# Kernel tuning notes

Measured on AMD Instinct MI355X. Metric: run time of the kernel, lower is better.

Reference implementation:

```python
import jax, jax.numpy as jnp
import numpy as np
import math

B, S, D, H = 2, 2048, 1024, 16
DK = D // H


def setup_inputs() -> dict:
    key = jax.random.key(0)
    ks = jax.random.split(key, 12)
    std = 1.0 / math.sqrt(D)
    inp = {
        "query": jax.random.normal(ks[0], (B, S, D), jnp.float32),
        "key": jax.random.normal(ks[1], (B, S, D), jnp.float32),
        "value": jax.random.normal(ks[2], (B, S, D), jnp.float32),
        # causal mask, broadcast over batch and heads
        "mask": jnp.tril(jnp.ones((S, S), jnp.int32))[None, None, :, :],
        # nn.Linear weights are [out_features, in_features]
        "Wq": jax.random.uniform(ks[3], (D, D), jnp.float32, -std, std),
        "bq": jax.random.uniform(ks[4], (D,), jnp.float32, -std, std),
        "Wk": jax.random.uniform(ks[5], (D, D), jnp.float32, -std, std),
        "bk": jax.random.uniform(ks[6], (D,), jnp.float32, -std, std),
        "Wv": jax.random.uniform(ks[7], (D, D), jnp.float32, -std, std),
        "bv": jax.random.uniform(ks[8], (D,), jnp.float32, -std, std),
        "Wo": jax.random.uniform(ks[9], (D, D), jnp.float32, -std, std),
        "bo": jax.random.uniform(ks[10], (D,), jnp.float32, -std, std),
    }
    return inp


def reference(query, key, value, mask, Wq, bq, Wk, bk, Wv, bv, Wo, bo):
    q = query @ Wq.T + bq  # [B,S,D]
    k = key @ Wk.T + bk
    v = value @ Wv.T + bv
    # Faithful to the original: a raw view (reshape), NOT a head-transpose split.
    q = q.reshape(B, H, S, DK)
    k = k.reshape(B, H, S, DK)
    v = v.reshape(B, H, S, DK)
    scores = jnp.einsum("bhqd,bhkd->bhqk", q, k) / math.sqrt(DK)
    scores = jnp.where(mask == 0, jnp.float32(-1e9), scores)
    weights = jax.nn.softmax(scores, axis=-1)
    # dropout(p=0.1) is identity in eval mode
    context = jnp.einsum("bhqk,bhkd->bhqd", weights, v)
    context = context.transpose(0, 2, 1, 3).reshape(B, S, D)
    return context @ Wo.T + bo
```

## Files before the change

### kernel.cpp

```cpp
#include <hip/hip_runtime.h>
#include <hip/hip_bf16.h>

#define BB 2
#define SS 2048
#define DD 1024
#define HH 16
#define DKK 64

typedef __attribute__((ext_vector_type(4))) float  f32x4;
typedef __attribute__((ext_vector_type(8))) short  s16x8;
typedef __attribute__((ext_vector_type(4))) short  s16x4;
typedef __attribute__((ext_vector_type(4))) float  fvec4;
typedef __attribute__((ext_vector_type(2))) unsigned int u32x2;
typedef __attribute__((ext_vector_type(4))) unsigned int u32x4;

__device__ __forceinline__ short f2bs(float f) {
    union { __hip_bfloat16 b; short s; } u;
    u.b = __float2bfloat16(f);
    return u.s;
}

__device__ __forceinline__ unsigned cvtpk(float lo, float hi) {
    unsigned r;
    asm("v_cvt_pk_bf16_f32 %0, %1, %2" : "=v"(r) : "v"(lo), "v"(hi));
    return r;
}

__device__ __forceinline__ void gload_lds16(const short* g, short* l) {
    __builtin_amdgcn_global_load_lds((const __attribute__((address_space(1))) void*)g,
                                     (__attribute__((address_space(3))) void*)l, 16, 0, 0);
}

__global__ __launch_bounds__(256) void cvt_w(
    const float* __restrict__ wq, const float* __restrict__ wk,
    const float* __restrict__ wv, const float* __restrict__ wo,
    short* __restrict__ wqo, short* __restrict__ wko,
    short* __restrict__ wvo, short* __restrict__ woo)
{
    const float* src; short* dst;
    switch (blockIdx.y) {
        case 0: src = wq; dst = wqo; break;
        case 1: src = wk; dst = wko; break;
        case 2: src = wv; dst = wvo; break;
        default: src = wo; dst = woo; break;
    }
    const int n = DD * DD;
    int i = (blockIdx.x * 256 + threadIdx.x) * 8;
    const int stride = gridDim.x * 256 * 8;
    for (; i < n; i += stride) {
        fvec4 a = *(const fvec4*)&src[i];
        fvec4 b = *(const fvec4*)&src[i + 4];
        s16x8 o;
        o[0] = f2bs(a[0]); o[1] = f2bs(a[1]); o[2] = f2bs(a[2]); o[3] = f2bs(a[3]);
        o[4] = f2bs(b[0]); o[5] = f2bs(b[1]); o[6] = f2bs(b[2]); o[7] = f2bs(b[3]);
        *(s16x8*)&dst[i] = o;
    }
}

template<int BN, int NXSH, bool OUTF32, bool AF32>
__global__ __launch_bounds__(256) void gemm_nt_v2(
    const void* __restrict__ A0, const void* __restrict__ A1, const void* __restrict__ A2,
    const short* __restrict__ B0, const short* __restrict__ B1, const short* __restrict__ B2,
    const float* __restrict__ c0, const float* __restrict__ c1, const float* __restrict__ c2,
    void* __restrict__ O0, void* __restrict__ O1, void* __restrict__ O2,
    float os0, float os1, float os2,
    int ppx, int NY, int KL, int N, int K)
{
    const int d   = blockIdx.x;
    const int xcd = d & 7;
    const int s   = d >> 3;
    const int x   = s & ((1 << NXSH) - 1);
    const int pl  = s >> NXSH;
    const int panel = xcd * ppx + pl;
    const int y   = panel % NY;
    const int z   = panel / NY;

    const void* Av    = z == 0 ? A0 : (z == 1 ? A1 : A2);
    const short* Bw   = z == 0 ? B0 : (z == 1 ? B1 : B2);
    const float* bias = z == 0 ? c0 : (z == 1 ? c1 : c2);
    void* Cp          = z == 0 ? O0 : (z == 1 ? O1 : O2);
    const float oscale = z == 0 ? os0 : (z == 1 ? os1 : os2);
    const short* Ab = (const short*)Av;
    const float* Af = (const float*)Av;

    __shared__ short As[128][64];
    __shared__ short Bs[BN][64];

    const int tid  = threadIdx.x;
    const int lane = tid & 63;
    const int wid  = tid >> 6;
    const int r16  = lane & 15;
    const int g    = lane >> 4;
    const int m0   = y * 128;
    const int n0   = x * BN;
    constexpr int MR = 4;
    constexpr int NR = BN / 32;
    const int wr   = (wid >> 1) * 64;
    const int wc   = (wid & 1) * (BN / 2);
    const int srow8 = lane >> 3;
    const int c8    = lane & 7;

    f32x4 acc[MR][NR];
#pragma unroll
    for (int mi = 0; mi < MR; ++mi)
#pragma unroll
        for (int ni = 0; ni < NR; ++ni) acc[mi][ni] = (f32x4){0.f, 0.f, 0.f, 0.f};

    const int csrc = (c8 ^ srow8) * 8;
    const int nk = KL >> 6;
#pragma unroll 1
    for (int kt = 0; kt < nk; ++kt) {
        const int k0 = kt * 64;
        if (kt) __syncthreads();
#pragma unroll
        for (int q = 0; q < BN / 32; ++q) {
            const int r = wid * (BN / 4) + q * 8 + srow8;
            gload_lds16(&Bw[(size_t)(n0 + r) * K + k0 + csrc], &Bs[wid * (BN / 4) + q * 8][0]);
        }
        if constexpr (AF32) {
#pragma unroll
            for (int it = 0; it < 4; ++it) {
                const int idx = it * 256 + tid;
                const int row = idx >> 3;
                const int ca  = idx & 7;
                const float* srcp = &Af[(size_t)(m0 + row) * K + k0 + ca * 8];
                const fvec4 a0 = *(const fvec4*)srcp;
                const fvec4 a1 = *(const fvec4*)(srcp + 4);
                u32x4 wv_;
                wv_[0] = cvtpk(a0[0], a0[1]);
                wv_[1] = cvtpk(a0[2], a0[3]);
                wv_[2] = cvtpk(a1[0], a1[1]);
                wv_[3] = cvtpk(a1[2], a1[3]);
                *(u32x4*)&As[row][((ca ^ (row & 7)) & 7) * 8] = wv_;
            }
        } else {
#pragma unroll
            for (int q = 0; q < 4; ++q) {
                const int r = wid * 32 + q * 8 + srow8;
                gload_lds16(&Ab[(size_t)(m0 + r) * K + k0 + csrc], &As[wid * 32 + q * 8][0]);
            }
        }
        __syncthreads();

#pragma unroll
        for (int kk = 0; kk < 2; ++kk) {
            s16x8 af[MR], bf[NR];
#pragma unroll
            for (int mi = 0; mi < MR; ++mi) {
                const int row = wr + mi * 16 + r16;
                af[mi] = *(const s16x8*)&As[row][((kk * 4 + g) ^ (row & 7)) * 8];
            }
#pragma unroll
            for (int ni = 0; ni < NR; ++ni) {
                const int row = wc + ni * 16 + r16;
                bf[ni] = *(const s16x8*)&Bs[row][((kk * 4 + g) ^ (row & 7)) * 8];
            }
#pragma unroll
            for (int mi = 0; mi < MR; ++mi)
#pragma unroll
                for (int ni = 0; ni < NR; ++ni)
                    acc[mi][ni] = __builtin_amdgcn_mfma_f32_16x16x32_bf16(
                        bf[ni], af[mi], acc[mi][ni], 0, 0, 0);
        }
    }

#pragma unroll
    for (int mi = 0; mi < MR; ++mi) {
        const size_t row = (size_t)(m0 + wr + mi * 16 + r16);
#pragma unroll
        for (int ni = 0; ni < NR; ++ni) {
            const int colb = n0 + wc + ni * 16 + g * 4;
            fvec4 bv;
            if (bias) bv = *(const fvec4*)&bias[colb];
            else      bv = (fvec4){0.f, 0.f, 0.f, 0.f};
            const f32x4 a = acc[mi][ni];
            const float v0 = (a[0] + bv[0]) * oscale;
            const float v1 = (a[1] + bv[1]) * oscale;
            const float v2 = (a[2] + bv[2]) * oscale;
            const float v3 = (a[3] + bv[3]) * oscale;
            if constexpr (OUTF32) {
                fvec4 o; o[0] = v0; o[1] = v1; o[2] = v2; o[3] = v3;
                *(fvec4*)&((float*)Cp)[row * N + colb] = o;
            } else {
                u32x2 w;
                w[0] = cvtpk(v0, v1);
                w[1] = cvtpk(v2, v3);
                *(u32x2*)&((short*)Cp)[row * N + colb] = w;
            }
        }
    }
}

__global__ __launch_bounds__(256) void mha_transpose_v(
    const short* __restrict__ vp, short* __restrict__ vT)
{
    const int st = blockIdx.x;
    const int bh = blockIdx.y;
    const short* src = vp + (size_t)bh * SS * DKK;
    short*       dst = vT + (size_t)bh * SS * DKK;
    const int tid = threadIdx.x;
#pragma unroll
    for (int i = 0; i < 2; ++i) {
        const int c  = tid + i * 256;
        const int dk = c >> 3;
        const int sc = c & 7;
        const int s0 = st * 64 + sc * 8;
        s16x8 v;
#pragma unroll
        for (int j = 0; j < 8; ++j) v[j] = src[(size_t)(s0 + j) * DKK + dk];
        *(s16x8*)&dst[(size_t)dk * SS + s0] = v;
    }
}

__global__ __launch_bounds__(256, 2) void mha_attn(
    const short* __restrict__ qp, const short* __restrict__ kp,
    const short* __restrict__ vT, short* __restrict__ ctx)
{
    __shared__ short Ks[64][64];
    __shared__ short Vs[64][64];
    __shared__ short P[4][16][72];

    const int tid  = threadIdx.x;
    const int wid  = tid >> 6;
    const int lane = tid & 63;
    const int r16  = lane & 15;
    const int g    = lane >> 4;

    const int lin = blockIdx.x;
    const int xcd = lin & 7;
    const int s8  = lin >> 3;
    const int bh  = (xcd << 2) | (s8 & 3);
    const int v   = s8 >> 2;
    const int grp = (v < 16) ? v : (47 - v);
    const int b   = bh >> 4;
    const int h   = bh & 15;

    const short* Qh = qp + (size_t)bh * SS * DKK;
    const short* Kh = kp + (size_t)bh * SS * DKK;
    const short* Vh = vT + (size_t)bh * SS * DKK;

    const int srow = lane >> 3;
    const int csw  = (((lane & 7) ^ srow) & 7) * 8;
    const int r0   = wid * 16;

    const int qr0 = grp * 64 + wid * 16;
    const int nkt = grp + 1;

    const s16x8 qf0 = *(const s16x8*)&Qh[(size_t)(qr0 + r16) * DKK + g * 8];
    const s16x8 qf1 = *(const s16x8*)&Qh[(size_t)(qr0 + r16) * DKK + 32 + g * 8];

    f32x4 po[4];
#pragma unroll
    for (int i = 0; i < 4; ++i) po[i] = (f32x4){0.f, 0.f, 0.f, 0.f};
    float lsum = 0.f;

#pragma unroll 1
    for (int j = 0; j < nkt; ++j) {
        const int k0 = j * 64;
        __syncthreads();
        {
            const int rowA = r0 + srow;
            const int rowB = rowA + 8;
            gload_lds16(&Kh[(size_t)(k0 + rowA) * DKK + csw], &Ks[r0][0]);
            gload_lds16(&Kh[(size_t)(k0 + rowB) * DKK + csw], &Ks[r0 + 8][0]);
            gload_lds16(&Vh[(size_t)rowA * SS + k0 + csw], &Vs[r0][0]);
            gload_lds16(&Vh[(size_t)rowB * SS + k0 + csw], &Vs[r0 + 8][0]);
        }
        __syncthreads();

        f32x4 sc[4];
        __builtin_amdgcn_s_setprio(1);
#pragma unroll
        for (int cg = 0; cg < 4; ++cg) {
            const int R  = cg * 16 + r16;
            const int sw = R & 7;
            const s16x8 kf0 = *(const s16x8*)&Ks[R][((g ^ sw) & 7) * 8];
            const s16x8 kf1 = *(const s16x8*)&Ks[R][(((4 + g) ^ sw) & 7) * 8];
            f32x4 tt = (f32x4){0.f, 0.f, 0.f, 0.f};
            tt = __builtin_amdgcn_mfma_f32_16x16x32_bf16(kf0, qf0, tt, 0, 0, 0);
            tt = __builtin_amdgcn_mfma_f32_16x16x32_bf16(kf1, qf1, tt, 0, 0, 0);
            sc[cg] = tt;
        }
        __builtin_amdgcn_s_setprio(0);

        if (j == nkt - 1) {
#pragma unroll
            for (int cg = 0; cg < 4; ++cg)
#pragma unroll
                for (int r = 0; r < 4; ++r)
                    if (k0 + cg * 16 + g * 4 + r > qr0 + r16) sc[cg][r] = -1e9f;
        }
#pragma unroll
        for (int cg = 0; cg < 4; ++cg) {
            const float p0 = __expf(sc[cg][0]);
            const float p1 = __expf(sc[cg][1]);
            const float p2 = __expf(sc[cg][2]);
            const float p3 = __expf(sc[cg][3]);
            lsum += (p0 + p1) + (p2 + p3);
            u32x2 w;
            w[0] = cvtpk(p0, p1);
            w[1] = cvtpk(p2, p3);
            *(u32x2*)&P[wid][r16][cg * 16 + g * 4] = w;
        }
        const s16x8 pf0 = *(const s16x8*)&P[wid][r16][g * 8];
        const s16x8 pf1 = *(const s16x8*)&P[wid][r16][32 + g * 8];

        __builtin_amdgcn_s_setprio(1);
#pragma unroll
        for (int dg = 0; dg < 4; ++dg) {
            const int Rv = dg * 16 + r16;
            const int sw = Rv & 7;
            const s16x8 vf0 = *(const s16x8*)&Vs[Rv][((g ^ sw) & 7) * 8];
            const s16x8 vf1 = *(const s16x8*)&Vs[Rv][(((4 + g) ^ sw) & 7) * 8];
            po[dg] = __builtin_amdgcn_mfma_f32_16x16x32_bf16(pf0, vf0, po[dg], 0, 0, 0);
            po[dg] = __builtin_amdgcn_mfma_f32_16x16x32_bf16(pf1, vf1, po[dg], 0, 0, 0);
        }
        __builtin_amdgcn_s_setprio(0);
    }

    lsum += __shfl_xor(lsum, 16);
    lsum += __shfl_xor(lsum, 32);
    const float linv = __builtin_amdgcn_rcpf(lsum);
    float rowinv[4];
#pragma unroll
    for (int r = 0; r < 4; ++r)
        rowinv[r] = __shfl(linv, g * 4 + r);
#pragma unroll
    for (int dg = 0; dg < 4; ++dg)
#pragma unroll
        for (int r = 0; r < 4; ++r) {
            const int srw = qr0 + g * 4 + r;
            const float vv = po[dg][r] * rowinv[r];
            ctx[((size_t)(b * SS + srw)) * DD + h * 64 + dg * 16 + r16] = f2bs(vv);
        }
}

extern "C" void kernel_launch(void* const* d_in, const int* in_sizes, int n_in,
                              void* d_out, int out_size, void* d_ws, size_t ws_size,
                              hipStream_t stream) {
    const float* query = (const float*)d_in[0];
    const float* key   = (const float*)d_in[1];
    const float* value = (const float*)d_in[2];
    const float* Wq = (const float*)d_in[4];
    const float* bq = (const float*)d_in[5];
    const float* Wk = (const float*)d_in[6];
    const float* bk = (const float*)d_in[7];
    const float* Wv = (const float*)d_in[8];
    const float* bv = (const float*)d_in[9];
    const float* Wo = (const float*)d_in[10];
    const float* bo = (const float*)d_in[11];
    float* out = (float*)d_out;

    const size_t elems = (size_t)BB * SS * DD;
    const size_t wel   = (size_t)DD * DD;
    short* wqx = (short*)d_ws;
    short* wkx = wqx + wel;
    short* wvx = wkx + wel;
    short* wox = wvx + wel;
    short* qp  = wox + wel;
    short* kp  = qp + elems;
    short* vp  = kp + elems;
    short* vT  = vp + elems;
    short* ctx = vT + elems;

    cvt_w<<<dim3(512, 4), 256, 0, stream>>>(Wq, Wk, Wv, Wo, wqx, wkx, wvx, wox);
    gemm_nt_v2<128, 3, false, true><<<dim3(768), 256, 0, stream>>>(
        query, key, value, wqx, wkx, wvx, bq, bk, bv, qp, kp, vp,
        0.125f, 1.0f, 1.0f, 12, 32, 1024, DD, DD);
    mha_transpose_v<<<dim3(SS / 64, BB * HH), 256, 0, stream>>>(vp, vT);
    mha_attn<<<dim3(1024), 256, 0, stream>>>(qp, kp, vT, ctx);
    gemm_nt_v2<64, 4, true, false><<<dim3(512), 256, 0, stream>>>(
        ctx, ctx, ctx, wox, wox, wox, bo, bo, bo, out, out, out,
        1.0f, 1.0f, 1.0f, 4, 32, 1024, DD, DD);
}
```

Before: 114.2 us.

## Prefetch next fp32 A tile into registers during MFMA in projection GEMM

In the fp32-input GEMM path, global loads of the next K-tile of A are issued before the current tile's MFMA work, and the bf16 conversion runs after it. This overlaps global latency with compute instead of stalling on loads each iteration. The syncthreads calls are replaced by manual waitcnt and s_barrier calls with sched barriers, which adds register pressure and relies on the vmcnt counting being correct.

```diff
diff --git a/kernel.cpp b/kernel.cpp
--- a/kernel.cpp
+++ b/kernel.cpp
@@ -108,59 +108,126 @@
 
     const int csrc = (c8 ^ srow8) * 8;
     const int nk = KL >> 6;
+
+    if constexpr (AF32) {
+        const int brow = tid >> 3;
+        const int ca   = tid & 7;
+        const int cswA = ((ca ^ (brow & 7)) & 7) * 8;
+
+        fvec4 la0[4], la1[4];
+        u32x4 areg[4];
+
+#pragma unroll
+        for (int it = 0; it < 4; ++it) {
+            const float* sp = &Af[(size_t)(m0 + brow + it * 32) * K + ca * 8];
+            la0[it] = *(const fvec4*)sp;
+            la1[it] = *(const fvec4*)(sp + 4);
+        }
+#pragma unroll
+        for (int it = 0; it < 4; ++it) {
+            areg[it][0] = cvtpk(la0[it][0], la0[it][1]);
+            areg[it][1] = cvtpk(la0[it][2], la0[it][3]);
+            areg[it][2] = cvtpk(la1[it][0], la1[it][1]);
+            areg[it][3] = cvtpk(la1[it][2], la1[it][3]);
+        }
+
 #pragma unroll 1
-    for (int kt = 0; kt < nk; ++kt) {
-        const int k0 = kt * 64;
-        if (kt) __syncthreads();
-#pragma unroll
-        for (int q = 0; q < BN / 32; ++q) {
-            const int r = wid * (BN / 4) + q * 8 + srow8;
-            gload_lds16(&Bw[(size_t)(n0 + r) * K + k0 + csrc], &Bs[wid * (BN / 4) + q * 8][0]);
-        }
-        if constexpr (AF32) {
-#pragma unroll
-            for (int it = 0; it < 4; ++it) {
-                const int idx = it * 256 + tid;
-                const int row = idx >> 3;
-                const int ca  = idx & 7;
-                const float* srcp = &Af[(size_t)(m0 + row) * K + k0 + ca * 8];
-                const fvec4 a0 = *(const fvec4*)srcp;
-                const fvec4 a1 = *(const fvec4*)(srcp + 4);
-                u32x4 wv_;
-                wv_[0] = cvtpk(a0[0], a0[1]);
-                wv_[1] = cvtpk(a0[2], a0[3]);
-                wv_[2] = cvtpk(a1[0], a1[1]);
-                wv_[3] = cvtpk(a1[2], a1[3]);
-                *(u32x4*)&As[row][((ca ^ (row & 7)) & 7) * 8] = wv_;
-            }
-        } else {
+        for (int kt = 0; kt < nk; ++kt) {
+            const int k0 = kt * 64;
+#pragma unroll
+            for (int it = 0; it < 4; ++it)
+                *(u32x4*)&As[brow + it * 32][cswA] = areg[it];
+#pragma unroll
+            for (int q = 0; q < BN / 32; ++q) {
+                const int r = wid * (BN / 4) + q * 8 + srow8;
+                gload_lds16(&Bw[(size_t)(n0 + r) * K + k0 + csrc], &Bs[wid * (BN / 4) + q * 8][0]);
+            }
+            const bool hasNext = (kt + 1 < nk);
+            if (hasNext) {
+                const int k1 = k0 + 64;
+#pragma unroll
+                for (int it = 0; it < 4; ++it) {
+                    const float* sp = &Af[(size_t)(m0 + brow + it * 32) * K + k1 + ca * 8];
+                    la0[it] = *(const fvec4*)sp;
+                    la1[it] = *(const fvec4*)(sp + 4);
+                }
+                asm volatile("s_waitcnt vmcnt(8) lgkmcnt(0)" ::: "memory");
+            } else {
+                asm volatile("s_waitcnt vmcnt(0) lgkmcnt(0)" ::: "memory");
+            }
+            __builtin_amdgcn_s_barrier();
+            __builtin_amdgcn_sched_barrier(0);
+
+#pragma unroll
+            for (int kk = 0; kk < 2; ++kk) {
+                s16x8 af[MR], bf[NR];
+#pragma unroll
+                for (int mi = 0; mi < MR; ++mi) {
+                    const int row = wr + mi * 16 + r16;
+                    af[mi] = *(const s16x8*)&As[row][((kk * 4 + g) ^ (row & 7)) * 8];
+                }
+#pragma unroll
+                for (int ni = 0; ni < NR; ++ni) {
+                    const int row = wc + ni * 16 + r16;
+                    bf[ni] = *(const s16x8*)&Bs[row][((kk * 4 + g) ^ (row & 7)) * 8];
+                }
+#pragma unroll
+                for (int mi = 0; mi < MR; ++mi)
+#pragma unroll
+                    for (int ni = 0; ni < NR; ++ni)
+                        acc[mi][ni] = __builtin_amdgcn_mfma_f32_16x16x32_bf16(
+                            bf[ni], af[mi], acc[mi][ni], 0, 0, 0);
+            }
+            if (hasNext) {
+#pragma unroll
+                for (int it = 0; it < 4; ++it) {
+                    areg[it][0] = cvtpk(la0[it][0], la0[it][1]);
+                    areg[it][1] = cvtpk(la0[it][2], la0[it][3]);
+                    areg[it][2] = cvtpk(la1[it][0], la1[it][1]);
+                    areg[it][3] = cvtpk(la1[it][2], la1[it][3]);
+                }
+            }
+            __builtin_amdgcn_sched_barrier(0);
+            asm volatile("s_waitcnt lgkmcnt(0)" ::: "memory");
+            __builtin_amdgcn_s_barrier();
+        }
+    } else {
+#pragma unroll 1
+        for (int kt = 0; kt < nk; ++kt) {
+            const int k0 = kt * 64;
+            if (kt) __syncthreads();
 #pragma unroll
             for (int q = 0; q < 4; ++q) {
                 const int r = wid * 32 + q * 8 + srow8;
                 gload_lds16(&Ab[(size_t)(m0 + r) * K + k0 + csrc], &As[wid * 32 + q * 8][0]);
             }
-        }
-        __syncthreads();
-
-#pragma unroll
-        for (int kk = 0; kk < 2; ++kk) {
-            s16x8 af[MR], bf[NR];
-#pragma unroll
-            for (int mi = 0; mi < MR; ++mi) {
-                const int row = wr + mi * 16 + r16;
-                af[mi] = *(const s16x8*)&As[row][((kk * 4 + g) ^ (row & 7)) * 8];
-            }
-#pragma unroll
-            for (int ni = 0; ni < NR; ++ni) {
-                const int row = wc + ni * 16 + r16;
-                bf[ni] = *(const s16x8*)&Bs[row][((kk * 4 + g) ^ (row & 7)) * 8];
-            }
-#pragma unroll
-            for (int mi = 0; mi < MR; ++mi)
-#pragma unroll
-                for (int ni = 0; ni < NR; ++ni)
-                    acc[mi][ni] = __builtin_amdgcn_mfma_f32_16x16x32_bf16(
-                        bf[ni], af[mi], acc[mi][ni], 0, 0, 0);
+#pragma unroll
+            for (int q = 0; q < BN / 32; ++q) {
+                const int r = wid * (BN / 4) + q * 8 + srow8;
+                gload_lds16(&Bw[(size_t)(n0 + r) * K + k0 + csrc], &Bs[wid * (BN / 4) + q * 8][0]);
+            }
+            __syncthreads();
+
+#pragma unroll
+            for (int kk = 0; kk < 2; ++kk) {
+                s16x8 af[MR], bf[NR];
+#pragma unroll
+                for (int mi = 0; mi < MR; ++mi) {
+                    const int row = wr + mi * 16 + r16;
+                    af[mi] = *(const s16x8*)&As[row][((kk * 4 + g) ^ (row & 7)) * 8];
+                }
+#pragma unroll
+                for (int ni = 0; ni < NR; ++ni) {
+                    const int row = wc + ni * 16 + r16;
+                    bf[ni] = *(const s16x8*)&Bs[row][((kk * 4 + g) ^ (row & 7)) * 8];
+                }
+#pragma unroll
+                for (int mi = 0; mi < MR; ++mi)
+#pragma unroll
+                    for (int ni = 0; ni < NR; ++ni)
+                        acc[mi][ni] = __builtin_amdgcn_mfma_f32_16x16x32_bf16(
+                            bf[ni], af[mi], acc[mi][ni], 0, 0, 0);
+            }
         }
     }
 
```

After: 121.7 us. 1.07x slower.
